# Performance work log

Hardware: AMD Instinct MI355X
Metric: run time of the kernel (lower is better)

## Reference

```python
import jax, jax.numpy as jnp
import numpy as np
import math

B, S, D, K = 8, 2048, 1024, 64
EPS = 1e-5

def _ln(x):
    m = jnp.mean(x, axis=-1, keepdims=True)
    v = jnp.mean((x - m) ** 2, axis=-1, keepdims=True)
    return (x - m) * jax.lax.rsqrt(v + EPS)

def setup_inputs() -> dict:
    key = jax.random.key(0)
    ks = jax.random.split(key, 14)
    s = 0.02
    return {
        "x":  jax.random.normal(ks[0], (B, S, D), dtype=jnp.float32),
        "Wk": jax.random.normal(ks[1], (D, K), dtype=jnp.float32) * s,
        "bk": jnp.zeros((K,), dtype=jnp.float32),
        "Wq": jax.random.normal(ks[2], (D, K), dtype=jnp.float32) * s,
        "bq": jnp.zeros((K,), dtype=jnp.float32),
        "Wv": jax.random.normal(ks[3], (D, D), dtype=jnp.float32) * s,
        "bv": jnp.zeros((D,), dtype=jnp.float32),
        "Wb": jax.random.normal(ks[4], (D, 1), dtype=jnp.float32) * s,
        "bb": jnp.zeros((1,), dtype=jnp.float32),
        "W1": jax.random.normal(ks[5], (D, D), dtype=jnp.float32) * s,
        "b1": jnp.zeros((D,), dtype=jnp.float32),
        "g1": jnp.ones((D,), dtype=jnp.float32),
        "be1": jnp.zeros((D,), dtype=jnp.float32),
    }

def reference(x, Wk, bk, Wq, bq, Wv, bv, Wb, bb, W1, b1, g1, be1):
    scale = 1.0 / math.sqrt(K)
    keys    = (jnp.einsum('bsd,dk->bsk', x, Wk) + bk) * scale   # [B,S,K]
    queries = jnp.einsum('bsd,dk->bsk', x, Wq) + bq             # [B,S,K]
    values  = jnp.einsum('bsd,de->bse', x, Wv) + bv             # [B,S,D]
    biases  = jnp.einsum('bsd,do->bso', x, Wb) + bb             # [B,S,1]
    # scores[b,i,j] = keys[b,i] . queries[b,j] + biases[b,i]
    scores = jax.nn.sigmoid(jnp.einsum('bik,bjk->bij', keys, queries) + biases)
    attention = jnp.einsum('bij,bjd->bid', scores, values)      # [B,S,D]
    res = _ln(x + attention) * g1 + be1
    feedforward = jax.nn.relu(jnp.einsum('bsd,de->bse', res, W1) + b1)
    return _ln(res + feedforward)
```

## Files before the change

kernel.cpp:

```cpp
#include <hip/hip_runtime.h>
#include <math.h>


typedef __bf16 bf16_t;
typedef __bf16 bf16x4_t __attribute__((ext_vector_type(4)));
typedef __bf16 bf16x8_t __attribute__((ext_vector_type(8)));
typedef float  f32x4    __attribute__((ext_vector_type(4)));

#define DEV static __device__ __forceinline__

DEV void gll16(const void* g, void* l) {
  __builtin_amdgcn_global_load_lds(
      (const __attribute__((address_space(1))) void*)g,
      (__attribute__((address_space(3))) void*)l, 16, 0, 0);
}

template <int MODE, int MFAST>
__global__ __launch_bounds__(512, 4) void gemm128n(
    const bf16_t* __restrict__ A, const bf16_t* __restrict__ B,
    bf16_t* __restrict__ C, int K, int lda, int ldb, int ldc,
    const float* __restrict__ aux0) {
  const int gx = gridDim.x, gy = gridDim.y;
  const int nwg = gx * gy;
  const int orig = blockIdx.x + gx * blockIdx.y;
  const int lid = (orig & 7) * (nwg >> 3) + (orig >> 3);
  const int bx = MFAST ? (lid / gy) : (lid % gx);
  const int by = MFAST ? (lid % gy) : (lid / gx);
  const int m0 = by * 256, n0 = bx * 128;

  __shared__ bf16_t SM[24576];
#define ASH(s) (&SM[(s) << 13])
#define BSH(s) (&SM[16384 + ((s) << 12)])

  const int tid = threadIdx.x;
  const int wid = tid >> 6, l = tid & 63;
  const int wr = wid >> 1, wc = wid & 1;
  const int lr = l & 15, lh = l >> 4;

  const int sRow = tid >> 2;
  const int sSl = (tid & 3) ^ ((tid >> 3) & 3);
  const bf16_t* Asrc = A + (long)(m0 + sRow) * lda + sSl * 8;
  const bf16_t* Bsrc = B + (long)(n0 + sRow) * ldb + sSl * 8;
  const long aStep = (long)128 * lda;

  const int sw = (lh ^ ((lr >> 1) & 3)) * 8;
  const int aOff = (wr * 64 + lr) * 32 + sw;
  const int bOff = (wc * 64 + lr) * 32 + sw;

  f32x4 acc[4][4] = {};
  const int NT = K >> 5;

  gll16(Asrc, ASH(0) + tid * 8);
  gll16(Asrc + aStep, ASH(0) + 4096 + tid * 8);
  gll16(Bsrc, BSH(0) + tid * 8);

  for (int h = 0; h < NT; ++h) {
    const int s = h & 1;
    asm volatile("s_waitcnt vmcnt(0)" ::: "memory");
    __builtin_amdgcn_sched_barrier(0);
    __builtin_amdgcn_s_barrier();
    if (h + 1 < NT) {
      const bf16_t* a_ = Asrc + (h + 1) * 32;
      const bf16_t* b_ = Bsrc + (h + 1) * 32;
      gll16(a_, ASH(s ^ 1) + tid * 8);
      gll16(a_ + aStep, ASH(s ^ 1) + 4096 + tid * 8);
      gll16(b_, BSH(s ^ 1) + tid * 8);
    }
    bf16x8_t aF[4], bF[4];
#pragma unroll
    for (int m = 0; m < 4; ++m) aF[m] = *(const bf16x8_t*)(ASH(s) + aOff + m * 512);
#pragma unroll
    for (int n = 0; n < 4; ++n) bF[n] = *(const bf16x8_t*)(BSH(s) + bOff + n * 512);
    asm volatile("s_waitcnt lgkmcnt(0)" ::: "memory");
    __builtin_amdgcn_sched_barrier(0);
    __builtin_amdgcn_s_setprio(1);
#pragma unroll
    for (int m = 0; m < 4; ++m)
#pragma unroll
      for (int n = 0; n < 4; ++n)
        acc[m][n] = __builtin_amdgcn_mfma_f32_16x16x32_bf16(aF[m], bF[n], acc[m][n], 0, 0, 0);
    __builtin_amdgcn_s_setprio(0);
  }

  const int rowb = m0 + wr * 64 + lh * 4;
  const int colb = n0 + wc * 64 + lr;
#pragma unroll
  for (int m = 0; m < 4; ++m)
#pragma unroll
    for (int n = 0; n < 4; ++n) {
      const f32x4 v = acc[m][n];
      const int cc = colb + n * 16;
#pragma unroll
      for (int r = 0; r < 4; ++r) {
        const int rr = rowb + m * 16 + r;
        const float val = v[r];
        if constexpr (MODE == 1) {
          C[(long)rr * ldc + cc] = (bf16_t)(val + aux0[rr]);
        } else {
          C[(long)rr * ldc + cc] = (bf16_t)fmaxf(val + aux0[cc], 0.0f);
        }
      }
    }
#undef ASH
#undef BSH
}

template <int MODE>
__global__ __launch_bounds__(512, 2) void gemm256p(
    const bf16_t* __restrict__ A, const bf16_t* __restrict__ B,
    bf16_t* __restrict__ C, int K, int lda, int ldb, int ldc,
    long sAb, long sBb, long sCb, const float* __restrict__ aux0) {
  const int gx = gridDim.x, gy = gridDim.y;
  const int gxy = gx * gy;
  const int nwg = gxy * (int)gridDim.z;
  const int orig = blockIdx.x + gx * blockIdx.y + gxy * blockIdx.z;
  const int lid = (orig & 7) * (nwg >> 3) + (orig >> 3);
  const int bz = lid / gxy;
  const int rem = lid - bz * gxy;
  const int bx = rem % gx;
  const int by = rem / gx;

  A += (long)bz * sAb;
  B += (long)bz * sBb;
  const int m0 = by * 256, n0 = bx * 256;

  __shared__ bf16_t SM[65536];
#define ASH(b, h) (&SM[(((b)*2 + (h)) << 13)])
#define BSH(b, h) (&SM[32768 + (((b)*2 + (h)) << 13)])

  const int tid = threadIdx.x;
  const int wid = tid >> 6, l = tid & 63;
  const int wr = wid >> 2, wc = wid & 3;
  const int lr = l & 15, lh = l >> 4;

  const int sRow = tid >> 2;
  const int sSl = (tid & 3) ^ ((tid >> 3) & 3);
  const bf16_t* Asrc = A + (long)(m0 + sRow) * lda + sSl * 8;
  const bf16_t* Bsrc = B + (long)(n0 + sRow) * ldb + sSl * 8;
  const long aStep = (long)128 * lda, bStep = (long)128 * ldb;

#define STAGE_A(b, h, kt) do { \
    const bf16_t* s_ = Asrc + (kt) * 64 + (h) * 32; \
    gll16(s_,         ASH(b, h) + tid * 8); \
    gll16(s_ + aStep, ASH(b, h) + 4096 + tid * 8); } while (0)
#define STAGE_B(b, h, kt) do { \
    const bf16_t* s_ = Bsrc + (kt) * 64 + (h) * 32; \
    gll16(s_,         BSH(b, h) + tid * 8); \
    gll16(s_ + bStep, BSH(b, h) + 4096 + tid * 8); } while (0)

  const int sw = (lh ^ ((lr >> 1) & 3)) * 8;
  const int aOff = (wr * 128 + lr) * 32 + sw;
  const int bOff = (wc * 64 + lr) * 32 + sw;

  f32x4 acc[8][4] = {};
  const int NT = K >> 6;

#define LGKM(n) do { \
    asm volatile("s_waitcnt lgkmcnt(" #n ")" ::: "memory"); \
    __builtin_amdgcn_sched_barrier(0); } while (0)
#define MFMA16(AS, BS, mo) do { \
    __builtin_amdgcn_s_setprio(1); \
    _Pragma("unroll") for (int m = 0; m < 4; ++m) \
    _Pragma("unroll") for (int n = 0; n < 4; ++n) \
      acc[m + (mo)][n] = __builtin_amdgcn_mfma_f32_16x16x32_bf16(AS[m], BS[n], acc[m + (mo)][n], 0, 0, 0); \
    __builtin_amdgcn_s_setprio(0); } while (0)

  STAGE_A(0, 0, 0); STAGE_B(0, 0, 0); STAGE_A(0, 1, 0); STAGE_B(0, 1, 0);
  asm volatile("s_waitcnt vmcnt(4)" ::: "memory");
  __builtin_amdgcn_s_barrier();

  bf16x8_t aA[4], aB[4], bA[4], bB[4];
#pragma unroll
  for (int n = 0; n < 4; ++n) bA[n] = *(const bf16x8_t*)(BSH(0, 0) + bOff + n * 512);
#pragma unroll
  for (int m = 0; m < 4; ++m) aA[m] = *(const bf16x8_t*)(ASH(0, 0) + aOff + m * 512);

  for (int t = 0; t < NT; ++t) {
    const int p = t & 1, q = p ^ 1;
    const bool pf = (t + 1 < NT);

#pragma unroll
    for (int m = 0; m < 4; ++m) aB[m] = *(const bf16x8_t*)(ASH(p, 0) + aOff + (m + 4) * 512);
    if (pf) STAGE_A(q, 0, t + 1);
    LGKM(4);
    MFMA16(aA, bA, 0);

    if (pf) {
      asm volatile("s_waitcnt vmcnt(2)" ::: "memory");
    } else {
      asm volatile("s_waitcnt vmcnt(0)" ::: "memory");
    }
    __builtin_amdgcn_sched_barrier(0);
    __builtin_amdgcn_s_barrier();
#pragma unroll
    for (int m = 0; m < 4; ++m) aA[m] = *(const bf16x8_t*)(ASH(p, 1) + aOff + m * 512);
#pragma unroll
    for (int n = 0; n < 4; ++n) bB[n] = *(const bf16x8_t*)(BSH(p, 1) + bOff + n * 512);
    if (pf) STAGE_B(q, 0, t + 1);
    LGKM(8);
    MFMA16(aB, bA, 4);

#pragma unroll
    for (int m = 0; m < 4; ++m) aB[m] = *(const bf16x8_t*)(ASH(p, 1) + aOff + (m + 4) * 512);
    if (pf) STAGE_A(q, 1, t + 1);
    LGKM(4);
    MFMA16(aA, bB, 0);

    if (pf) STAGE_B(q, 1, t + 1);
    asm volatile("s_waitcnt lgkmcnt(0)" ::: "memory");
    if (pf) {
      asm volatile("s_waitcnt vmcnt(4)" ::: "memory");
    }
    __builtin_amdgcn_sched_barrier(0);
    __builtin_amdgcn_s_barrier();
    if (pf) {
#pragma unroll
      for (int n = 0; n < 4; ++n) bA[n] = *(const bf16x8_t*)(BSH(q, 0) + bOff + n * 512);
#pragma unroll
      for (int m = 0; m < 4; ++m) aA[m] = *(const bf16x8_t*)(ASH(q, 0) + aOff + m * 512);
    }
    __builtin_amdgcn_sched_barrier(0);
    MFMA16(aB, bB, 4);
  }
#undef STAGE_A
#undef STAGE_B
#undef LGKM
#undef MFMA16

  bf16_t* Cb = C + (long)bz * sCb;
  const int rowb = m0 + wr * 128 + lh * 4;
  const int colb = n0 + wc * 64 + lr;
#pragma unroll
  for (int m = 0; m < 8; ++m)
#pragma unroll
    for (int n = 0; n < 4; ++n) {
      const f32x4 v = acc[m][n];
      const int cc = colb + n * 16;
#pragma unroll
      for (int r = 0; r < 4; ++r) {
        const int rr = rowb + m * 16 + r;
        Cb[(long)rr * ldc + cc] = (bf16_t)v[r];
      }
    }
#undef ASH
#undef BSH
}

__global__ __launch_bounds__(256) void scores128(
    const bf16_t* __restrict__ kq, bf16_t* __restrict__ C,
    const float* __restrict__ biases) {
  const int orig = blockIdx.x + 16 * blockIdx.y + 256 * blockIdx.z;
  const int lid = (orig & 7) * 256 + (orig >> 3);
  const int bz = lid >> 8;
  const int rem = lid & 255;
  const int bx = rem & 15, by = rem >> 4;

  const bf16_t* A = kq + (long)bz * 2048 * 128;
  const bf16_t* B = A + 64;
  const float* a0 = biases + (long)bz * 2048;
  const int m0 = by * 128, n0 = bx * 128;

  __shared__ bf16_t SM[16384];
#define ASH(h) (&SM[(h) << 12])
#define BSH(h) (&SM[8192 + ((h) << 12)])

  const int tid = threadIdx.x;
  const int w = tid >> 6, l = tid & 63;
  const int wr = w >> 1, wc = w & 1;
  const int lr = l & 15, lh = l >> 4;

  const int sRow = tid >> 2;
  const int sSl = ((tid & 3) ^ ((tid >> 3) & 3)) * 8;
  const bf16_t* As = A + (long)(m0 + sRow) * 128 + sSl;
  const bf16_t* Bs = B + (long)(n0 + sRow) * 128 + sSl;
#pragma unroll
  for (int h = 0; h < 2; ++h) {
    gll16(As + h * 32, ASH(h) + tid * 8);
    gll16(As + h * 32 + 64 * 128, ASH(h) + 2048 + tid * 8);
    gll16(Bs + h * 32, BSH(h) + tid * 8);
    gll16(Bs + h * 32 + 64 * 128, BSH(h) + 2048 + tid * 8);
  }
  asm volatile("s_waitcnt vmcnt(0)" ::: "memory");
  __builtin_amdgcn_s_barrier();

  const int sw = (lh ^ ((lr >> 1) & 3)) * 8;
  const int aOff = (wr * 64 + lr) * 32 + sw;
  const int bOff = (wc * 64 + lr) * 32 + sw;

  f32x4 acc[4][4] = {};
#pragma unroll
  for (int h = 0; h < 2; ++h) {
    bf16x8_t aF[4], bF[4];
#pragma unroll
    for (int m = 0; m < 4; ++m) aF[m] = *(const bf16x8_t*)(ASH(h) + aOff + m * 512);
#pragma unroll
    for (int n = 0; n < 4; ++n) bF[n] = *(const bf16x8_t*)(BSH(h) + bOff + n * 512);
#pragma unroll
    for (int m = 0; m < 4; ++m)
#pragma unroll
      for (int n = 0; n < 4; ++n)
        acc[m][n] = __builtin_amdgcn_mfma_f32_16x16x32_bf16(aF[m], bF[n], acc[m][n], 0, 0, 0);
  }

  __builtin_amdgcn_s_barrier();
  {
    const int rowb = (wr << 6) + (lh << 2);
    const int colb = (wc << 6) + lr;
#pragma unroll
    for (int m = 0; m < 4; ++m)
#pragma unroll
      for (int n = 0; n < 4; ++n) {
        const f32x4 v = acc[m][n];
        const int cl = colb + (n << 4);
#pragma unroll
        for (int r = 0; r < 4; ++r) {
          const int rl = rowb + (m << 4) + r;
          const float zz = v[r] + a0[m0 + rl];
          SM[rl * 128 + (cl ^ (lh << 4))] =
              (bf16_t)__builtin_amdgcn_rcpf(1.0f + __expf(-zz));
        }
      }
    __syncthreads();
    bf16_t* Cb = C + (long)bz * 2048 * 2048;
    const int chunk = tid & 15, rsub = tid >> 4;
#pragma unroll
    for (int pp = 0; pp < 8; ++pp) {
      const int rl = pp * 16 + rsub;
      const int sc = chunk ^ (((rl >> 2) & 3) << 1);
      const bf16x8_t vv = *(const bf16x8_t*)&SM[rl * 128 + sc * 8];
      *(bf16x8_t*)&Cb[(long)(m0 + rl) * 2048 + n0 + chunk * 8] = vv;
    }
  }
#undef ASH
#undef BSH
}

__global__ __launch_bounds__(256) void kq_thin(
    const bf16_t* __restrict__ A, const bf16_t* __restrict__ B,
    bf16_t* __restrict__ C,
    const float* __restrict__ bk, const float* __restrict__ bq) {
  const int m0 = blockIdx.x * 64;

  __shared__ bf16_t SM[12288];
#define ASH(b) (&SM[(b) << 11])
#define BSH(b) (&SM[4096 + ((b) << 12)])

  const int tid = threadIdx.x;
  const int w = tid >> 6, l = tid & 63;
  const int lr = l & 15, lh = l >> 4;

  const int sRow = tid >> 2;
  const int sSl = (tid & 3) ^ ((tid >> 3) & 3);
  const bf16_t* Asrc = A + (long)(m0 + sRow) * 1024 + sSl * 8;
  const bf16_t* Bsrc0 = B + (long)sRow * 1024 + sSl * 8;
  const bf16_t* Bsrc1 = B + (long)(64 + sRow) * 1024 + sSl * 8;

  const int sw = (lh ^ ((lr >> 1) & 3)) * 8;
  const int aOff = (w * 16 + lr) * 32 + sw;

  f32x4 acc[8] = {};

  auto stage = [&](int buf, int k0) {
    gll16(Asrc + k0, ASH(buf) + tid * 8);
    gll16(Bsrc0 + k0, BSH(buf) + tid * 8);
    gll16(Bsrc1 + k0, BSH(buf) + 2048 + tid * 8);
  };

  stage(0, 0);
  for (int h = 0; h < 32; ++h) {
    const int s = h & 1;
    asm volatile("s_waitcnt vmcnt(0)" ::: "memory");
    __builtin_amdgcn_sched_barrier(0);
    __builtin_amdgcn_s_barrier();
    if (h + 1 < 32) stage(s ^ 1, (h + 1) * 32);

    const bf16x8_t aF = *(const bf16x8_t*)(ASH(s) + aOff);
    bf16x8_t bF[8];
#pragma unroll
    for (int j = 0; j < 8; ++j)
      bF[j] = *(const bf16x8_t*)(BSH(s) + (j * 16 + lr) * 32 + sw);
    asm volatile("s_waitcnt lgkmcnt(0)" ::: "memory");
    __builtin_amdgcn_sched_barrier(0);
    __builtin_amdgcn_s_setprio(1);
#pragma unroll
    for (int j = 0; j < 8; ++j)
      acc[j] = __builtin_amdgcn_mfma_f32_16x16x32_bf16(aF, bF[j], acc[j], 0, 0, 0);
    __builtin_amdgcn_s_setprio(0);
  }

  {
#pragma unroll
    for (int j = 0; j < 8; ++j) {
      const f32x4 v = acc[j];
      const int cl = j * 16 + lr;
      const float b = (cl < 64) ? bk[cl] : bq[cl - 64];
      const float s = (cl < 64) ? 0.125f : 1.0f;
#pragma unroll
      for (int r = 0; r < 4; ++r) {
        const int rl = w * 16 + lh * 4 + r;
        SM[rl * 128 + (cl ^ (lh << 4))] = (bf16_t)((v[r] + b) * s);
      }
    }
    __syncthreads();
    const int chunk = tid & 15, rsub = tid >> 4;
#pragma unroll
    for (int pp = 0; pp < 4; ++pp) {
      const int rl = pp * 16 + rsub;
      const int sc = chunk ^ (((rl >> 2) & 3) << 1);
      const bf16x8_t vv = *(const bf16x8_t*)&SM[rl * 128 + sc * 8];
      *(bf16x8_t*)&C[(long)(m0 + rl) * 128 + chunk * 8] = vv;
    }
  }
#undef ASH
#undef BSH
}

__global__ __launch_bounds__(256) void prep(
    const float* __restrict__ x, const float* __restrict__ Wb,
    const float* __restrict__ bb, bf16_t* __restrict__ x_bf,
    float* __restrict__ biases,
    const float* __restrict__ Wk, const float* __restrict__ Wq,
    const float* __restrict__ Wv, const float* __restrict__ W1,
    bf16_t* __restrict__ Wkqt, bf16_t* __restrict__ Wvt,
    bf16_t* __restrict__ W1t) {
  __shared__ float t[32][33];
  if (blockIdx.x < 4096) {
    const int r = blockIdx.x * 4 + (threadIdx.x >> 6);
    const int l = threadIdx.x & 63;
    const float* xr = x + (long)r * 1024;
    bf16_t* orow = x_bf + (long)r * 1024;
    float s = 0.f;
#pragma unroll
    for (int i = 0; i < 4; ++i) {
      const int off = l * 4 + i * 256;
      const float4 v = *(const float4*)(xr + off);
      const float4 w = *(const float4*)(Wb + off);
      s += v.x * w.x + v.y * w.y + v.z * w.z + v.w * w.w;
      bf16x4_t o;
      o[0] = (bf16_t)v.x; o[1] = (bf16_t)v.y; o[2] = (bf16_t)v.z; o[3] = (bf16_t)v.w;
      *(bf16x4_t*)(orow + off) = o;
    }
#pragma unroll
    for (int off = 1; off < 64; off <<= 1) s += __shfl_xor(s, off);
    if (l == 0) biases[r] = s + bb[0];
    return;
  }
  int b = blockIdx.x - 4096;
  const float* in;
  bf16_t* out;
  int R = 1024, C, c0, r0;
  if (b < 1024) {
    in = Wv; out = Wvt; C = 1024;
    c0 = (b & 31) * 32; r0 = (b >> 5) * 32;
  } else if (b < 2048) {
    b -= 1024; in = W1; out = W1t; C = 1024;
    c0 = (b & 31) * 32; r0 = (b >> 5) * 32;
  } else if (b < 2112) {
    b -= 2048; in = Wk; out = Wkqt; C = 64;
    c0 = (b & 1) * 32; r0 = (b >> 1) * 32;
  } else {
    b -= 2112; in = Wq; out = Wkqt + 64 * 1024; C = 64;
    c0 = (b & 1) * 32; r0 = (b >> 1) * 32;
  }
  const int tx = threadIdx.x & 31, ty = threadIdx.x >> 5;
#pragma unroll
  for (int i = 0; i < 4; ++i) {
    const int rl = ty * 4 + i;
    t[rl][tx] = in[(long)(r0 + rl) * C + c0 + tx];
  }
  __syncthreads();
#pragma unroll
  for (int i = 0; i < 4; ++i) {
    const int rl = ty * 4 + i;
    out[(long)(c0 + rl) * R + r0 + tx] = (bf16_t)t[tx][rl];
  }
}

__global__ __launch_bounds__(256) void ln1_kernel(
    const bf16_t* __restrict__ x, const bf16_t* __restrict__ attn,
    const float* __restrict__ g, const float* __restrict__ be,
    bf16_t* __restrict__ res) {
  const int w = threadIdx.x >> 6, l = threadIdx.x & 63;
  const long r = (long)blockIdx.x * 4 + w;
  const bf16_t* xr = x + r * 1024;
  const bf16_t* ar = attn + r * 1024;
  float y[16];
  float s = 0.f, ss = 0.f;
#pragma unroll
  for (int h = 0; h < 2; ++h) {
    const int base = h * 512 + l * 8;
    const bf16x8_t xv = *(const bf16x8_t*)(xr + base);
    const bf16x8_t av = *(const bf16x8_t*)(ar + base);
#pragma unroll
    for (int j = 0; j < 8; ++j) {
      const float yy = (float)xv[j] + (float)av[j];
      y[h * 8 + j] = yy;
      s += yy; ss += yy * yy;
    }
  }
#pragma unroll
  for (int off = 1; off < 64; off <<= 1) {
    s += __shfl_xor(s, off);
    ss += __shfl_xor(ss, off);
  }
  const float mean = s * (1.0f / 1024.0f);
  const float rs = rsqrtf(ss * (1.0f / 1024.0f) - mean * mean + 1e-5f);
  bf16_t* orow = res + r * 1024;
#pragma unroll
  for (int h = 0; h < 2; ++h) {
    const int base = h * 512 + l * 8;
    bf16x8_t o;
#pragma unroll
    for (int j = 0; j < 8; ++j)
      o[j] = (bf16_t)((y[h * 8 + j] - mean) * rs * g[base + j] + be[base + j]);
    *(bf16x8_t*)(orow + base) = o;
  }
}

__global__ __launch_bounds__(256) void ln2_kernel(
    const bf16_t* __restrict__ res, const bf16_t* __restrict__ hh,
    float* __restrict__ out) {
  const int w = threadIdx.x >> 6, l = threadIdx.x & 63;
  const long r = (long)blockIdx.x * 4 + w;
  const bf16_t* rr = res + r * 1024;
  const bf16_t* hr = hh + r * 1024;
  float y[16];
  float s = 0.f, ss = 0.f;
#pragma unroll
  for (int h = 0; h < 2; ++h) {
    const int base = h * 512 + l * 8;
    const bf16x8_t rv = *(const bf16x8_t*)(rr + base);
    const bf16x8_t hv = *(const bf16x8_t*)(hr + base);
#pragma unroll
    for (int j = 0; j < 8; ++j) {
      const float yy = (float)rv[j] + (float)hv[j];
      y[h * 8 + j] = yy;
      s += yy; ss += yy * yy;
    }
  }
#pragma unroll
  for (int off = 1; off < 64; off <<= 1) {
    s += __shfl_xor(s, off);
    ss += __shfl_xor(ss, off);
  }
  const float mean = s * (1.0f / 1024.0f);
  const float rs = rsqrtf(ss * (1.0f / 1024.0f) - mean * mean + 1e-5f);
  float* orow = out + r * 1024;
#pragma unroll
  for (int h = 0; h < 2; ++h) {
    const int base = h * 512 + l * 8;
    float4 o1, o2;
    o1.x = (y[h * 8 + 0] - mean) * rs; o1.y = (y[h * 8 + 1] - mean) * rs;
    o1.z = (y[h * 8 + 2] - mean) * rs; o1.w = (y[h * 8 + 3] - mean) * rs;
    o2.x = (y[h * 8 + 4] - mean) * rs; o2.y = (y[h * 8 + 5] - mean) * rs;
    o2.z = (y[h * 8 + 6] - mean) * rs; o2.w = (y[h * 8 + 7] - mean) * rs;
    *(float4*)(orow + base) = o1;
    *(float4*)(orow + base + 4) = o2;
  }
}

extern "C" void kernel_launch(void* const* d_in, const int* in_sizes, int n_in,
                              void* d_out, int out_size, void* d_ws, size_t ws_size,
                              hipStream_t stream) {
  const float* x   = (const float*)d_in[0];
  const float* Wk  = (const float*)d_in[1];
  const float* bk  = (const float*)d_in[2];
  const float* Wq  = (const float*)d_in[3];
  const float* bq  = (const float*)d_in[4];
  const float* Wv  = (const float*)d_in[5];
  const float* bv  = (const float*)d_in[6];
  const float* Wb  = (const float*)d_in[7];
  const float* bb  = (const float*)d_in[8];
  const float* W1  = (const float*)d_in[9];
  const float* b1  = (const float*)d_in[10];
  const float* g1  = (const float*)d_in[11];
  const float* be1 = (const float*)d_in[12];
  float* out = (float*)d_out;

  char* ws = (char*)d_ws;
  bf16_t* x_bf    = (bf16_t*)(ws + 0);
  bf16_t* vt_bf   = (bf16_t*)(ws + 33554432);
  bf16_t* kq_bf   = (bf16_t*)(ws + 67108864);
  bf16_t* Wkqt    = (bf16_t*)(ws + 71303168);
  bf16_t* Wvt     = (bf16_t*)(ws + 71565312);
  bf16_t* W1t     = (bf16_t*)(ws + 73662464);
  float*  biases  = (float*) (ws + 75759616);
  bf16_t* scores  = (bf16_t*)(ws + 75825152);
  bf16_t* attn_bf = (bf16_t*)(ws + 142934016);
  bf16_t* res_bf  = (bf16_t*)(ws + 176488448);
  bf16_t* h_bf    = attn_bf;

  prep<<<6272, 256, 0, stream>>>(x, Wb, bb, x_bf, biases,
                                 Wk, Wq, Wv, W1, Wkqt, Wvt, W1t);

  kq_thin<<<256, 256, 0, stream>>>(x_bf, Wkqt, kq_bf, bk, bq);

  gemm128n<1, 1><<<dim3(128, 4), 512, 0, stream>>>(
      Wvt, x_bf, vt_bf, 1024, 1024, 1024, 16384, bv);

  scores128<<<dim3(16, 16, 8), 256, 0, stream>>>(kq_bf, scores, biases);

  gemm256p<3><<<dim3(4, 8, 8), 512, 0, stream>>>(
      scores, vt_bf, attn_bf, 2048, 2048, 16384, 1024,
      2048L * 2048, 2048, 2048L * 1024, nullptr);

  ln1_kernel<<<4096, 256, 0, stream>>>(x_bf, attn_bf, g1, be1, res_bf);

  gemm128n<4, 0><<<dim3(8, 64), 512, 0, stream>>>(
      res_bf, W1t, h_bf, 1024, 1024, 1024, 1024, b1);

  ln2_kernel<<<4096, 256, 0, stream>>>(res_bf, h_bf, out);
}
```

Baseline: 233.3 us.

## Merge K/Q projection and V-transpose GEMM into one launch

```diff
diff --git a/kernel.cpp b/kernel.cpp
--- a/kernel.cpp
+++ b/kernel.cpp
@@ -13,6 +13,155 @@
   __builtin_amdgcn_global_load_lds(
       (const __attribute__((address_space(1))) void*)g,
       (__attribute__((address_space(3))) void*)l, 16, 0, 0);
+}
+
+__global__ __launch_bounds__(512, 4) void vt_kq(
+    const bf16_t* __restrict__ Wvt, const bf16_t* __restrict__ x_bf,
+    bf16_t* __restrict__ vt, const float* __restrict__ bv,
+    const bf16_t* __restrict__ Wkqt, bf16_t* __restrict__ kqO,
+    const float* __restrict__ bk, const float* __restrict__ bq) {
+  __shared__ bf16_t SM[24576];
+  const int tid = threadIdx.x;
+  const int wid = tid >> 6, l = tid & 63;
+  const int lr = l & 15, lh = l >> 4;
+  const int sw = (lh ^ ((lr >> 1) & 3)) * 8;
+
+  if (blockIdx.x < 512) {
+#define ASH(s) (&SM[(s) << 13])
+#define BSH(s) (&SM[16384 + ((s) << 12)])
+    const int nwg = 512;
+    const int orig = blockIdx.x;
+    const int lid = (orig & 7) * (nwg >> 3) + (orig >> 3);
+    const int bx = lid / 4;
+    const int by = lid % 4;
+    const int m0 = by * 256, n0 = bx * 128;
+    const int lda = 1024, ldb = 1024, ldc = 16384;
+
+    const int wr = wid >> 1, wc = wid & 1;
+    const int sRow = tid >> 2;
+    const int sSl = (tid & 3) ^ ((tid >> 3) & 3);
+    const bf16_t* Asrc = Wvt + (long)(m0 + sRow) * lda + sSl * 8;
+    const bf16_t* Bsrc = x_bf + (long)(n0 + sRow) * ldb + sSl * 8;
+    const long aStep = (long)128 * lda;
+
+    const int aOff = (wr * 64 + lr) * 32 + sw;
+    const int bOff = (wc * 64 + lr) * 32 + sw;
+
+    f32x4 acc[4][4] = {};
+
+    gll16(Asrc, ASH(0) + tid * 8);
+    gll16(Asrc + aStep, ASH(0) + 4096 + tid * 8);
+    gll16(Bsrc, BSH(0) + tid * 8);
+
+    for (int h = 0; h < 32; ++h) {
+      const int s = h & 1;
+      asm volatile("s_waitcnt vmcnt(0)" ::: "memory");
+      __builtin_amdgcn_sched_barrier(0);
+      __builtin_amdgcn_s_barrier();
+      if (h + 1 < 32) {
+        const bf16_t* a_ = Asrc + (h + 1) * 32;
+        const bf16_t* b_ = Bsrc + (h + 1) * 32;
+        gll16(a_, ASH(s ^ 1) + tid * 8);
+        gll16(a_ + aStep, ASH(s ^ 1) + 4096 + tid * 8);
+        gll16(b_, BSH(s ^ 1) + tid * 8);
+      }
+      bf16x8_t aF[4], bF[4];
+#pragma unroll
+      for (int m = 0; m < 4; ++m) aF[m] = *(const bf16x8_t*)(ASH(s) + aOff + m * 512);
+#pragma unroll
+      for (int n = 0; n < 4; ++n) bF[n] = *(const bf16x8_t*)(BSH(s) + bOff + n * 512);
+      asm volatile("s_waitcnt lgkmcnt(0)" ::: "memory");
+      __builtin_amdgcn_sched_barrier(0);
+      __builtin_amdgcn_s_setprio(1);
+#pragma unroll
+      for (int m = 0; m < 4; ++m)
+#pragma unroll
+        for (int n = 0; n < 4; ++n)
+          acc[m][n] = __builtin_amdgcn_mfma_f32_16x16x32_bf16(aF[m], bF[n], acc[m][n], 0, 0, 0);
+      __builtin_amdgcn_s_setprio(0);
+    }
+
+    const int rowb = m0 + wr * 64 + lh * 4;
+    const int colb = n0 + wc * 64 + lr;
+#pragma unroll
+    for (int m = 0; m < 4; ++m)
+#pragma unroll
+      for (int n = 0; n < 4; ++n) {
+        const f32x4 v = acc[m][n];
+        const int cc = colb + n * 16;
+#pragma unroll
+        for (int r = 0; r < 4; ++r) {
+          const int rr = rowb + m * 16 + r;
+          vt[(long)rr * ldc + cc] = (bf16_t)(v[r] + bv[rr]);
+        }
+      }
+#undef ASH
+#undef BSH
+  } else {
+#define ASH(s) (&SM[(s) << 12])
+#define BSH(s) (&SM[8192 + ((s) << 12)])
+    const int m0 = (blockIdx.x - 512) * 128;
+
+    const int sRow = tid >> 2;
+    const int sSl = (tid & 3) ^ ((tid >> 3) & 3);
+    const bf16_t* Asrc = x_bf + (long)(m0 + sRow) * 1024 + sSl * 8;
+    const bf16_t* Bsrc = Wkqt + (long)sRow * 1024 + sSl * 8;
+
+    const int aOff = (wid * 16 + lr) * 32 + sw;
+
+    f32x4 acc[8] = {};
+
+    gll16(Asrc, ASH(0) + tid * 8);
+    gll16(Bsrc, BSH(0) + tid * 8);
+
+    for (int h = 0; h < 32; ++h) {
+      const int s = h & 1;
+      asm volatile("s_waitcnt vmcnt(0)" ::: "memory");
+      __builtin_amdgcn_sched_barrier(0);
+      __builtin_amdgcn_s_barrier();
+      if (h + 1 < 32) {
+        gll16(Asrc + (h + 1) * 32, ASH(s ^ 1) + tid * 8);
+        gll16(Bsrc + (h + 1) * 32, BSH(s ^ 1) + tid * 8);
+      }
+      const bf16x8_t aF = *(const bf16x8_t*)(ASH(s) + aOff);
+      bf16x8_t bF[8];
+#pragma unroll
+      for (int j = 0; j < 8; ++j)
+        bF[j] = *(const bf16x8_t*)(BSH(s) + (j * 16 + lr) * 32 + sw);
+      asm volatile("s_waitcnt lgkmcnt(0)" ::: "memory");
+      __builtin_amdgcn_sched_barrier(0);
+      __builtin_amdgcn_s_setprio(1);
+#pragma unroll
+      for (int j = 0; j < 8; ++j)
+        acc[j] = __builtin_amdgcn_mfma_f32_16x16x32_bf16(aF, bF[j], acc[j], 0, 0, 0);
+      __builtin_amdgcn_s_setprio(0);
+    }
+
+    __builtin_amdgcn_s_barrier();
+#pragma unroll
+    for (int j = 0; j < 8; ++j) {
+      const f32x4 v = acc[j];
+      const int cl = j * 16 + lr;
+      const float b = (cl < 64) ? bk[cl] : bq[cl - 64];
+      const float sc = (cl < 64) ? 0.125f : 1.0f;
+#pragma unroll
+      for (int r = 0; r < 4; ++r) {
+        const int rl = wid * 16 + lh * 4 + r;
+        SM[rl * 128 + (cl ^ (lh << 4))] = (bf16_t)((v[r] + b) * sc);
+      }
+    }
+    __builtin_amdgcn_s_barrier();
+    const int chunk = tid & 15, rsub = tid >> 4;
+#pragma unroll
+    for (int pp = 0; pp < 4; ++pp) {
+      const int rl = pp * 32 + rsub;
+      const int sc = chunk ^ (((rl >> 2) & 3) << 1);
+      const bf16x8_t vv = *(const bf16x8_t*)&SM[rl * 128 + sc * 8];
+      *(bf16x8_t*)&kqO[(long)(m0 + rl) * 128 + chunk * 8] = vv;
+    }
+#undef ASH
+#undef BSH
+  }
 }
 
 template <int MODE, int MFAST>
@@ -329,86 +478,6 @@
       const int sc = chunk ^ (((rl >> 2) & 3) << 1);
       const bf16x8_t vv = *(const bf16x8_t*)&SM[rl * 128 + sc * 8];
       *(bf16x8_t*)&Cb[(long)(m0 + rl) * 2048 + n0 + chunk * 8] = vv;
-    }
-  }
-#undef ASH
-#undef BSH
-}
-
-__global__ __launch_bounds__(256) void kq_thin(
-    const bf16_t* __restrict__ A, const bf16_t* __restrict__ B,
-    bf16_t* __restrict__ C,
-    const float* __restrict__ bk, const float* __restrict__ bq) {
-  const int m0 = blockIdx.x * 64;
-
-  __shared__ bf16_t SM[12288];
-#define ASH(b) (&SM[(b) << 11])
-#define BSH(b) (&SM[4096 + ((b) << 12)])
-
-  const int tid = threadIdx.x;
-  const int w = tid >> 6, l = tid & 63;
-  const int lr = l & 15, lh = l >> 4;
-
-  const int sRow = tid >> 2;
-  const int sSl = (tid & 3) ^ ((tid >> 3) & 3);
-  const bf16_t* Asrc = A + (long)(m0 + sRow) * 1024 + sSl * 8;
-  const bf16_t* Bsrc0 = B + (long)sRow * 1024 + sSl * 8;
-  const bf16_t* Bsrc1 = B + (long)(64 + sRow) * 1024 + sSl * 8;
-
-  const int sw = (lh ^ ((lr >> 1) & 3)) * 8;
-  const int aOff = (w * 16 + lr) * 32 + sw;
-
-  f32x4 acc[8] = {};
-
-  auto stage = [&](int buf, int k0) {
-    gll16(Asrc + k0, ASH(buf) + tid * 8);
-    gll16(Bsrc0 + k0, BSH(buf) + tid * 8);
-    gll16(Bsrc1 + k0, BSH(buf) + 2048 + tid * 8);
-  };
-
-  stage(0, 0);
-  for (int h = 0; h < 32; ++h) {
-    const int s = h & 1;
-    asm volatile("s_waitcnt vmcnt(0)" ::: "memory");
-    __builtin_amdgcn_sched_barrier(0);
-    __builtin_amdgcn_s_barrier();
-    if (h + 1 < 32) stage(s ^ 1, (h + 1) * 32);
-
-    const bf16x8_t aF = *(const bf16x8_t*)(ASH(s) + aOff);
-    bf16x8_t bF[8];
-#pragma unroll
-    for (int j = 0; j < 8; ++j)
-      bF[j] = *(const bf16x8_t*)(BSH(s) + (j * 16 + lr) * 32 + sw);
-    asm volatile("s_waitcnt lgkmcnt(0)" ::: "memory");
-    __builtin_amdgcn_sched_barrier(0);
-    __builtin_amdgcn_s_setprio(1);
-#pragma unroll
-    for (int j = 0; j < 8; ++j)
-      acc[j] = __builtin_amdgcn_mfma_f32_16x16x32_bf16(aF, bF[j], acc[j], 0, 0, 0);
-    __builtin_amdgcn_s_setprio(0);
-  }
-
-  {
-#pragma unroll
-    for (int j = 0; j < 8; ++j) {
-      const f32x4 v = acc[j];
-      const int cl = j * 16 + lr;
-      const float b = (cl < 64) ? bk[cl] : bq[cl - 64];
-      const float s = (cl < 64) ? 0.125f : 1.0f;
-#pragma unroll
-      for (int r = 0; r < 4; ++r) {
-        const int rl = w * 16 + lh * 4 + r;
-        SM[rl * 128 + (cl ^ (lh << 4))] = (bf16_t)((v[r] + b) * s);
-      }
-    }
-    __syncthreads();
-    const int chunk = tid & 15, rsub = tid >> 4;
-#pragma unroll
-    for (int pp = 0; pp < 4; ++pp) {
-      const int rl = pp * 16 + rsub;
-      const int sc = chunk ^ (((rl >> 2) & 3) << 1);
-      const bf16x8_t vv = *(const bf16x8_t*)&SM[rl * 128 + sc * 8];
-      *(bf16x8_t*)&C[(long)(m0 + rl) * 128 + chunk * 8] = vv;
     }
   }
 #undef ASH
@@ -593,10 +662,7 @@
   prep<<<6272, 256, 0, stream>>>(x, Wb, bb, x_bf, biases,
                                  Wk, Wq, Wv, W1, Wkqt, Wvt, W1t);
 
-  kq_thin<<<256, 256, 0, stream>>>(x_bf, Wkqt, kq_bf, bk, bq);
-
-  gemm128n<1, 1><<<dim3(128, 4), 512, 0, stream>>>(
-      Wvt, x_bf, vt_bf, 1024, 1024, 1024, 16384, bv);
+  vt_kq<<<640, 512, 0, stream>>>(Wvt, x_bf, vt_bf, bv, Wkqt, kq_bf, bk, bq);
 
   scores128<<<dim3(16, 16, 8), 256, 0, stream>>>(kq_bf, scores, biases);
 
```

After: 231.0 us, median of 2. No clear change (-1.0%).
